# Performance work log

Hardware: AMD Instinct MI355X
Metric: run time of the kernel (lower is better)

## Reference

```python
import jax, jax.numpy as jnp
import numpy as np

N = 50000   # nodes
E = 800000  # edges (avg degree 16)
F_IN = 128
H = 128
L = 4
LN_EPS = 1e-5


def setup_inputs() -> dict:
    key = jax.random.key(0)
    ks = jax.random.split(key, 4)
    x = jax.random.normal(ks[0], (N, F_IN), dtype=jnp.float32)
    edge_index = jax.random.randint(ks[1], (2, E), 0, N)
    conv_w = jax.random.normal(ks[2], (L, F_IN, H), dtype=jnp.float32) * 0.05
    conv_b = jnp.zeros((L, H), dtype=jnp.float32)
    ln_g = jnp.ones((L, H), dtype=jnp.float32)
    ln_b = jnp.zeros((L, H), dtype=jnp.float32)
    head_w = jax.random.normal(ks[3], (H, 1), dtype=jnp.float32) * 0.05
    head_b = jnp.zeros((1,), dtype=jnp.float32)
    return {"x": x, "edge_index": edge_index, "conv_w": conv_w, "conv_b": conv_b,
            "ln_g": ln_g, "ln_b": ln_b, "head_w": head_w, "head_b": head_b}


def _layer_norm(h, g, b):
    mu = jnp.mean(h, axis=-1, keepdims=True)
    var = jnp.mean(jnp.square(h - mu), axis=-1, keepdims=True)
    return (h - mu) * jax.lax.rsqrt(var + LN_EPS) * g + b


def _gcn_conv(h, W, b, src, dst, inv_sqrt_deg, inv_deg):
    # PyG GCNConv: self-loops + symmetric normalization D^-1/2 (A+I) D^-1/2, then bias.
    hw = h @ W  # (N, H)
    norm = inv_sqrt_deg[src] * inv_sqrt_deg[dst]  # (E,)
    msg = hw[src] * norm[:, None]  # gather + edgewise scale
    agg = jax.ops.segment_sum(msg, dst, num_segments=N)  # scatter-add
    agg = agg + hw * inv_deg[:, None]  # self-loop term (norm = 1/deg)
    return agg + b


def reference(x, edge_index, conv_w, conv_b, ln_g, ln_b, head_w, head_b):
    src, dst = edge_index[0], edge_index[1]
    # degree on target nodes, including self-loop
    deg = jax.ops.segment_sum(jnp.ones((E,), x.dtype), dst, num_segments=N) + 1.0
    inv_sqrt_deg = jax.lax.rsqrt(deg)
    inv_deg = 1.0 / deg
    h = x
    for i in range(L):
        h = _gcn_conv(h, conv_w[i], conv_b[i], src, dst, inv_sqrt_deg, inv_deg)
        h = _layer_norm(h, ln_g[i], ln_b[i])
        if i != L - 1:
            h = jax.nn.gelu(h, approximate=False)
            # dropout is identity in eval mode
    scores = (h @ head_w + head_b).squeeze(-1)  # (N,)
    return scores, h
```

## Files before the change

kernel.cpp:

```cpp
#include <hip/hip_runtime.h>
#include <math.h>

#define N_NODES 50000
#define N_EDGES 800000
#define HDIM 128
#define NLAYERS 4
#define LN_EPS 1e-5f
#define EQUARTER (N_EDGES / 4)
#define SEG 64
#define FILLB ((EQUARTER + 255) / 256)
#define GEMMB ((N_NODES + 63) / 64)
#define LFB ((N_NODES + 31) / 32)

typedef __attribute__((ext_vector_type(8))) short short8;
typedef __attribute__((ext_vector_type(4))) float floatx4;

__device__ __forceinline__ ushort f2bf(float x) {
    unsigned b = __float_as_uint(x);
    unsigned r = b + 0x7fffu + ((b >> 16) & 1u);
    return (ushort)(r >> 16);
}
__device__ __forceinline__ float2 bf2f2(unsigned u) {
    return make_float2(__uint_as_float(u << 16), __uint_as_float(u & 0xffff0000u));
}


__device__ __forceinline__ void fill_body(int bid, int tid, const int* __restrict__ src,
                                          const int* __restrict__ dst, int* __restrict__ cnt,
                                          ushort* __restrict__ csr16) {
    int t = bid * 256 + tid;
    if (t >= EQUARTER) return;
    int s0 = src[t],                d0 = dst[t];
    int s1 = src[t + EQUARTER],     d1 = dst[t + EQUARTER];
    int s2 = src[t + 2 * EQUARTER], d2 = dst[t + 2 * EQUARTER];
    int s3 = src[t + 3 * EQUARTER], d3 = dst[t + 3 * EQUARTER];
    int p0 = atomicAdd(&cnt[d0], 1);
    int p1 = atomicAdd(&cnt[d1], 1);
    int p2 = atomicAdd(&cnt[d2], 1);
    int p3 = atomicAdd(&cnt[d3], 1);
    if (p0 < SEG) csr16[d0 * SEG + p0] = (ushort)s0;
    if (p1 < SEG) csr16[d1 * SEG + p1] = (ushort)s1;
    if (p2 < SEG) csr16[d2 * SEG + p2] = (ushort)s2;
    if (p3 < SEG) csr16[d3 * SEG + p3] = (ushort)s3;
}

__global__ __launch_bounds__(256) void isd_kernel(const int* __restrict__ cnt,
                                                  float* __restrict__ isd,
                                                  float* __restrict__ ind) {
    int i = blockIdx.x * 256 + threadIdx.x;
    if (i < N_NODES) {
        float d = (float)cnt[i] + 1.0f;
        isd[i] = rsqrtf(d);
        ind[i] = 1.0f / d;
    }
}

__global__ __launch_bounds__(256) void bprep_kernel(const float* __restrict__ W,
                                                    ushort* __restrict__ bfrag) {
    int idx = blockIdx.x * 256 + threadIdx.x;
    if (idx >= NLAYERS * 4 * 8 * 64) return;
    int lane = idx & 63;
    int t = (idx >> 6) & 7;
    int s = (idx >> 9) & 3;
    int l = idx >> 11;
    int n = t * 16 + (lane & 15);
    int kb = s * 32 + (lane >> 4) * 8;
    const float* Wl = W + (size_t)l * HDIM * HDIM;
    union { uint4 q; ushort u[8]; } o;
#pragma unroll
    for (int j = 0; j < 8; ++j) o.u[j] = f2bf(Wl[(size_t)(kb + j) * HDIM + n]);
    *(uint4*)&bfrag[(size_t)idx * 8] = o.q;
}

template <bool A_FP32>
__device__ __forceinline__ void gemm_body(int bid, int tid, const void* __restrict__ Av,
                                          const ushort* __restrict__ bfrag,
                                          ushort* __restrict__ out) {
    int wave = tid >> 6, lane = tid & 63;
    int quad = lane >> 4, mrow = lane & 15;
    int rowBase = bid * 64 + wave * 16;
    int arow = rowBase + mrow;
    bool aok = arow < N_NODES;

    floatx4 acc[8];
#pragma unroll
    for (int t = 0; t < 8; ++t) acc[t] = (floatx4)0.f;

#pragma unroll
    for (int s = 0; s < 4; ++s) {
        union { short8 v; ushort u[8]; } af;
        if (A_FP32) {
            const float* A = (const float*)Av;
            if (aok) {
                const float* p = &A[(size_t)arow * HDIM + s * 32 + quad * 8];
#pragma unroll
                for (int j = 0; j < 8; ++j) af.u[j] = f2bf(p[j]);
            } else {
#pragma unroll
                for (int j = 0; j < 8; ++j) af.u[j] = 0;
            }
        } else {
            const ushort* A = (const ushort*)Av;
            if (aok) {
                af.v = *(const short8*)&A[(size_t)arow * HDIM + s * 32 + quad * 8];
            } else {
#pragma unroll
                for (int j = 0; j < 8; ++j) af.u[j] = 0;
            }
        }
#pragma unroll
        for (int t = 0; t < 8; ++t) {
            short8 bf = *(const short8*)&bfrag[(size_t)(((s * 8 + t) * 64) + lane) * 8];
            acc[t] = __builtin_amdgcn_mfma_f32_16x16x32_bf16(af.v, bf, acc[t], 0, 0, 0);
        }
    }
#pragma unroll
    for (int t = 0; t < 8; ++t) {
#pragma unroll
        for (int r = 0; r < 4; ++r) {
            int row = rowBase + quad * 4 + r;
            if (row < N_NODES) out[(size_t)row * HDIM + t * 16 + mrow] = f2bf(acc[t][r]);
        }
    }
}

__global__ __launch_bounds__(256) void fused0_kernel(
    const int* __restrict__ src, const int* __restrict__ dst, int* __restrict__ cnt,
    ushort* __restrict__ csr16, const float* __restrict__ x,
    const ushort* __restrict__ bfrag0, ushort* __restrict__ hw) {
    if (blockIdx.x < FILLB)
        fill_body(blockIdx.x, threadIdx.x, src, dst, cnt, csr16);
    else
        gemm_body<true>(blockIdx.x - FILLB, threadIdx.x, x, bfrag0, hw);
}

__global__ __launch_bounds__(256) void agg_ln_kernel(
    const uint2* __restrict__ hw2, const int* __restrict__ degcnt,
    const ushort* __restrict__ csr16, const float* __restrict__ isd,
    const float* __restrict__ ind, const float* __restrict__ conv_b,
    const float* __restrict__ ln_g, const float* __restrict__ ln_b,
    uint2* __restrict__ hout_bf, float* __restrict__ hout_f32,
    const float* __restrict__ head_w, const float* __restrict__ head_b,
    float* __restrict__ scores, int final_layer) {
    int wave = threadIdx.x >> 6;
    int lane = threadIdx.x & 63;
    int g = lane >> 5;
    int li = lane & 31;
    int n = blockIdx.x * 4 + wave;
    if (n >= N_NODES) return;
    int c = li * 4;

    float isd_n = isd[n], ind_n = ind[n];
    int rs = n * SEG;
    int deg = min(degcnt[n], SEG);

    float e0 = 0.f, e1 = 0.f, e2 = 0.f, e3 = 0.f;
    int sj = 0;
    float wj = 0.f;
    if (lane < deg) {
        sj = (int)csr16[rs + lane];
        wj = isd[sj];
    }
    for (int j = 0; j < deg; j += 8) {
#pragma unroll
        for (int t = 0; t < 4; ++t) {
            int idx = j + 2 * t + g;
            int s = __shfl(sj, idx);
            float w = __shfl(wj, idx);
            uint2 u = hw2[(size_t)s * 32 + li];
            float2 q0 = bf2f2(u.x), q1 = bf2f2(u.y);
            e0 = fmaf(q0.x, w, e0); e1 = fmaf(q0.y, w, e1);
            e2 = fmaf(q1.x, w, e2); e3 = fmaf(q1.y, w, e3);
        }
    }
    e0 += __shfl_xor(e0, 32); e1 += __shfl_xor(e1, 32);
    e2 += __shfl_xor(e2, 32); e3 += __shfl_xor(e3, 32);

    uint2 hv = hw2[(size_t)n * 32 + li];
    float2 h0 = bf2f2(hv.x), h1 = bf2f2(hv.y);
    float4 cb = *(const float4*)&conv_b[c];
    float a0 = fmaf(e0, isd_n, fmaf(h0.x, ind_n, cb.x));
    float a1 = fmaf(e1, isd_n, fmaf(h0.y, ind_n, cb.y));
    float a2 = fmaf(e2, isd_n, fmaf(h1.x, ind_n, cb.z));
    float a3 = fmaf(e3, isd_n, fmaf(h1.y, ind_n, cb.w));

    float sum = a0 + a1 + a2 + a3;
#pragma unroll
    for (int o = 1; o < 32; o <<= 1) sum += __shfl_xor(sum, o);
    float mu = sum * (1.0f / HDIM);
    float d0 = a0 - mu, d1 = a1 - mu, d2 = a2 - mu, d3 = a3 - mu;
    float vs = d0 * d0 + d1 * d1 + d2 * d2 + d3 * d3;
#pragma unroll
    for (int o = 1; o < 32; o <<= 1) vs += __shfl_xor(vs, o);
    float rstd = rsqrtf(vs * (1.0f / HDIM) + LN_EPS);
    float4 gv = *(const float4*)&ln_g[c];
    float4 bv = *(const float4*)&ln_b[c];
    float y0 = fmaf(d0 * rstd, gv.x, bv.x);
    float y1 = fmaf(d1 * rstd, gv.y, bv.y);
    float y2 = fmaf(d2 * rstd, gv.z, bv.z);
    float y3 = fmaf(d3 * rstd, gv.w, bv.w);

    if (!final_layer) {
#define GELU(v) ((v) = 0.5f * (v) * (1.0f + erff((v) * 0.70710678118654752f)))
        GELU(y0); GELU(y1); GELU(y2); GELU(y3);
#undef GELU
        if (g == 0) {
            uint2 ov;
            ov.x = (unsigned)f2bf(y0) | ((unsigned)f2bf(y1) << 16);
            ov.y = (unsigned)f2bf(y2) | ((unsigned)f2bf(y3) << 16);
            hout_bf[(size_t)n * 32 + li] = ov;
        }
    } else {
        if (g == 0)
            *(float4*)&hout_f32[(size_t)n * HDIM + c] = make_float4(y0, y1, y2, y3);
        float4 hwv = *(const float4*)&head_w[c];
        float p = y0 * hwv.x + y1 * hwv.y + y2 * hwv.z + y3 * hwv.w;
#pragma unroll
        for (int o = 1; o < 32; o <<= 1) p += __shfl_xor(p, o);
        if (lane == 0) scores[n] = p + head_b[0];
    }
}

__global__ __launch_bounds__(512) void layer_fused_kernel(
    const uint2* __restrict__ h2, const int* __restrict__ degcnt,
    const ushort* __restrict__ csr16, const float* __restrict__ isd,
    const float* __restrict__ ind, const ushort* __restrict__ bfrag,
    const float* __restrict__ conv_b, const float* __restrict__ ln_g,
    const float* __restrict__ ln_b, uint2* __restrict__ hout_bf,
    float* __restrict__ hout_f32, const float* __restrict__ head_w,
    const float* __restrict__ head_b, float* __restrict__ scores,
    int final_layer) {
    __shared__ float aggsf[32][132];
    int wave = threadIdx.x >> 6, lane = threadIdx.x & 63;
    int g = lane >> 5, li = lane & 31;

    int nodeBase = blockIdx.x * 32 + wave * 4;
    int deg_c = 0, sj_c = 0;
    float wj_c = 0.f;
    if (nodeBase < N_NODES) {
        deg_c = min(degcnt[nodeBase], SEG);
        int sraw = (int)csr16[nodeBase * SEG + lane];
        sj_c = (lane < deg_c) ? sraw : 0;
        float w = isd[sj_c];
        wj_c = (lane < deg_c) ? w : 0.f;
    }
    for (int it = 0; it < 4; ++it) {
        int n = nodeBase + it;
        int deg = deg_c, sj = sj_c;
        float wj = wj_c;
        int deg_nx = 0, sraw_nx = 0;
        if (it < 3 && (n + 1) < N_NODES) {
            deg_nx = min(degcnt[n + 1], SEG);
            sraw_nx = (int)csr16[(n + 1) * SEG + lane];
        }
        float a0 = 0.f, a1 = 0.f, a2 = 0.f, a3 = 0.f;
        if (n < N_NODES) {
            float isd_n = isd[n], ind_n = ind[n];
            uint2 hv = h2[(size_t)n * 32 + li];
            float e0 = 0.f, e1 = 0.f, e2 = 0.f, e3 = 0.f;
            uint2 u[4];
#pragma unroll
            for (int t = 0; t < 4; ++t) {
                int s = __shfl(sj, 2 * t + g);
                u[t] = h2[(size_t)s * 32 + li];
            }
            for (int j = 0; j < deg; j += 8) {
                uint2 un[4];
                int jn = j + 8;
                bool more = jn < deg;
                if (more) {
#pragma unroll
                    for (int t = 0; t < 4; ++t) {
                        int s = __shfl(sj, jn + 2 * t + g);
                        un[t] = h2[(size_t)s * 32 + li];
                    }
                }
#pragma unroll
                for (int t = 0; t < 4; ++t) {
                    float w = __shfl(wj, j + 2 * t + g);
                    float2 q0 = bf2f2(u[t].x), q1 = bf2f2(u[t].y);
                    e0 = fmaf(q0.x, w, e0); e1 = fmaf(q0.y, w, e1);
                    e2 = fmaf(q1.x, w, e2); e3 = fmaf(q1.y, w, e3);
                }
                if (more) { u[0] = un[0]; u[1] = un[1]; u[2] = un[2]; u[3] = un[3]; }
            }
            e0 += __shfl_xor(e0, 32); e1 += __shfl_xor(e1, 32);
            e2 += __shfl_xor(e2, 32); e3 += __shfl_xor(e3, 32);
            float2 h0 = bf2f2(hv.x), h1v = bf2f2(hv.y);
            a0 = fmaf(e0, isd_n, h0.x * ind_n);
            a1 = fmaf(e1, isd_n, h0.y * ind_n);
            a2 = fmaf(e2, isd_n, h1v.x * ind_n);
            a3 = fmaf(e3, isd_n, h1v.y * ind_n);
        }
        if (g == 0)
            *(float4*)&aggsf[wave * 4 + it][li * 4] = make_float4(a0, a1, a2, a3);
        deg_c = deg_nx;
        sj_c = (lane < deg_nx) ? sraw_nx : 0;
        float w = isd[sj_c];
        wj_c = (lane < deg_nx) ? w : 0.f;
    }
    __syncthreads();

    int quad = lane >> 4, mrow = lane & 15;
    int rtile = (wave >> 2) * 16;
    int cq2 = (wave & 3) * 2;
    floatx4 acc[2];
    acc[0] = (floatx4)0.f;
    acc[1] = (floatx4)0.f;
#pragma unroll
    for (int s = 0; s < 4; ++s) {
        const float* rowp = &aggsf[rtile + mrow][s * 32 + quad * 8];
        float4 pa = *(const float4*)rowp;
        float4 pb = *(const float4*)(rowp + 4);
        float p[8] = {pa.x, pa.y, pa.z, pa.w, pb.x, pb.y, pb.z, pb.w};
        union { short8 v; ushort u[8]; } hi, lo;
#pragma unroll
        for (int j = 0; j < 8; ++j) {
            ushort h = f2bf(p[j]);
            hi.u[j] = h;
            float hf = __uint_as_float((unsigned)h << 16);
            lo.u[j] = f2bf(p[j] - hf);
        }
#pragma unroll
        for (int t4 = 0; t4 < 2; ++t4) {
            int t = cq2 + t4;
            short8 bf = *(const short8*)&bfrag[(size_t)(((s * 8 + t) * 64) + lane) * 8];
            acc[t4] = __builtin_amdgcn_mfma_f32_16x16x32_bf16(lo.v, bf, acc[t4], 0, 0, 0);
            acc[t4] = __builtin_amdgcn_mfma_f32_16x16x32_bf16(hi.v, bf, acc[t4], 0, 0, 0);
        }
    }
    __syncthreads();

    {
        float cb[2];
#pragma unroll
        for (int t4 = 0; t4 < 2; ++t4) cb[t4] = conv_b[(cq2 + t4) * 16 + mrow];
#pragma unroll
        for (int t4 = 0; t4 < 2; ++t4)
#pragma unroll
            for (int r = 0; r < 4; ++r)
                aggsf[rtile + quad * 4 + r][(cq2 + t4) * 16 + mrow] = acc[t4][r] + cb[t4];
    }
    __syncthreads();

    int c = li * 4;
    float4 gv = *(const float4*)&ln_g[c];
    float4 bv = *(const float4*)&ln_b[c];
    float4 hwv = *(const float4*)&head_w[c];
    for (int it = 0; it < 4; ++it) {
        int row = wave * 4 + it;
        int n = blockIdx.x * 32 + row;
        if (n >= N_NODES) continue;
        float4 v = *(const float4*)&aggsf[row][c];
        float a0 = v.x, a1 = v.y, a2 = v.z, a3 = v.w;

        float sum = a0 + a1 + a2 + a3;
#pragma unroll
        for (int o = 1; o < 32; o <<= 1) sum += __shfl_xor(sum, o);
        float mu = sum * (1.0f / HDIM);
        float d0 = a0 - mu, d1 = a1 - mu, d2 = a2 - mu, d3 = a3 - mu;
        float vs = d0 * d0 + d1 * d1 + d2 * d2 + d3 * d3;
#pragma unroll
        for (int o = 1; o < 32; o <<= 1) vs += __shfl_xor(vs, o);
        float rstd = rsqrtf(vs * (1.0f / HDIM) + LN_EPS);
        float y0 = fmaf(d0 * rstd, gv.x, bv.x);
        float y1 = fmaf(d1 * rstd, gv.y, bv.y);
        float y2 = fmaf(d2 * rstd, gv.z, bv.z);
        float y3 = fmaf(d3 * rstd, gv.w, bv.w);

        if (!final_layer) {
#define GELU(v) ((v) = 0.5f * (v) * (1.0f + erff((v) * 0.70710678118654752f)))
            GELU(y0); GELU(y1); GELU(y2); GELU(y3);
#undef GELU
            if (g == 0) {
                uint2 ov;
                ov.x = (unsigned)f2bf(y0) | ((unsigned)f2bf(y1) << 16);
                ov.y = (unsigned)f2bf(y2) | ((unsigned)f2bf(y3) << 16);
                hout_bf[(size_t)n * 32 + li] = ov;
            }
        } else {
            if (g == 0)
                *(float4*)&hout_f32[(size_t)n * HDIM + c] = make_float4(y0, y1, y2, y3);
            float p = y0 * hwv.x + y1 * hwv.y + y2 * hwv.z + y3 * hwv.w;
#pragma unroll
            for (int o = 1; o < 32; o <<= 1) p += __shfl_xor(p, o);
            if (lane == 0) scores[n] = p + head_b[0];
        }
    }
}


extern "C" void kernel_launch(void* const* d_in, const int* in_sizes, int n_in,
                              void* d_out, int out_size, void* d_ws, size_t ws_size,
                              hipStream_t stream) {
    const float* x      = (const float*)d_in[0];
    const int*   eidx   = (const int*)d_in[1];
    const float* conv_w = (const float*)d_in[2];
    const float* conv_b = (const float*)d_in[3];
    const float* ln_g   = (const float*)d_in[4];
    const float* ln_b   = (const float*)d_in[5];
    const float* head_w = (const float*)d_in[6];
    const float* head_b = (const float*)d_in[7];
    float* out = (float*)d_out;

    const int* src = eidx;
    const int* dst = eidx + N_EDGES;

    char* ws = (char*)d_ws;
    size_t o = 0;
    auto alloc = [&](size_t elems) {
        void* p = ws + o * 4;
        o += (elems + 15) & ~(size_t)15;
        return p;
    };
    int*      cnt      = (int*)alloc(N_NODES);
    float*    isd      = (float*)alloc(N_NODES);
    float*    ind      = (float*)alloc(N_NODES);
    ushort*   csr16    = (ushort*)alloc((size_t)N_NODES * SEG / 2);
    ushort*   bfrag    = (ushort*)alloc(NLAYERS * 4 * 8 * 64 * 8 / 2);
    unsigned* hw       = (unsigned*)alloc((size_t)N_NODES * 64);
    unsigned* hbuf     = (unsigned*)alloc((size_t)N_NODES * 64);

    hipMemsetAsync(cnt, 0, N_NODES * sizeof(int), stream);
    bprep_kernel<<<(NLAYERS * 4 * 8 * 64 + 255) / 256, 256, 0, stream>>>(conv_w, bfrag);
    fused0_kernel<<<FILLB + GEMMB, 256, 0, stream>>>(src, dst, cnt, csr16, x, bfrag,
                                                     (ushort*)hw);
    isd_kernel<<<(N_NODES + 255) / 256, 256, 0, stream>>>(cnt, isd, ind);

    agg_ln_kernel<<<(N_NODES + 3) / 4, 256, 0, stream>>>(
        (const uint2*)hw, cnt, csr16, isd, ind,
        conv_b, ln_g, ln_b,
        (uint2*)hbuf, out + N_NODES, head_w, head_b, out, 0);

    const unsigned* hin = hbuf;
    unsigned* hnext = hw;
    for (int l = 1; l < NLAYERS; ++l) {
        const ushort* bl = bfrag + (size_t)l * 4 * 8 * 64 * 8;
        int fin = (l == NLAYERS - 1) ? 1 : 0;
        layer_fused_kernel<<<LFB, 512, 0, stream>>>(
            (const uint2*)hin, cnt, csr16, isd, ind, bl,
            conv_b + (size_t)l * HDIM, ln_g + (size_t)l * HDIM, ln_b + (size_t)l * HDIM,
            (uint2*)hnext, out + N_NODES, head_w, head_b, out, fin);
        const unsigned* tmp = hin;
        hin = hnext;
        hnext = (unsigned*)tmp;
    }
}
```

Before: 361.9 us.

## Fold memset and degree-norm kernels into prep and consumers, recompute rsqrt inline

Merges the memset of the count array with the weight-fragment prep kernel and removes the separate isd/ind kernel. The aggregation kernels now compute the inverse square root of degree directly from the raw counts. The edge-fill loop is also changed from four edges per thread to two. This cuts two launches and the isd/ind arrays, at the cost of extra rsqrt work in each layer's aggregation.

```diff
diff --git a/kernel.cpp b/kernel.cpp
--- a/kernel.cpp
+++ b/kernel.cpp
@@ -6,9 +6,9 @@
 #define HDIM 128
 #define NLAYERS 4
 #define LN_EPS 1e-5f
-#define EQUARTER (N_EDGES / 4)
+#define EHALF (N_EDGES / 2)
 #define SEG 64
-#define FILLB ((EQUARTER + 255) / 256)
+#define FILLB ((EHALF + 255) / 256)
 #define GEMMB ((N_NODES + 63) / 64)
 #define LFB ((N_NODES + 31) / 32)
 
@@ -24,52 +24,37 @@
     return make_float2(__uint_as_float(u << 16), __uint_as_float(u & 0xffff0000u));
 }
 
+__global__ __launch_bounds__(256) void prep_kernel(const float* __restrict__ W,
+                                                   ushort* __restrict__ bfrag,
+                                                   int* __restrict__ cnt) {
+    int idx = blockIdx.x * 256 + threadIdx.x;
+    if (idx < N_NODES) cnt[idx] = 0;
+    if (idx < NLAYERS * 4 * 8 * 64) {
+        int lane = idx & 63;
+        int t = (idx >> 6) & 7;
+        int s = (idx >> 9) & 3;
+        int l = idx >> 11;
+        int n = t * 16 + (lane & 15);
+        int kb = s * 32 + (lane >> 4) * 8;
+        const float* Wl = W + (size_t)l * HDIM * HDIM;
+        union { uint4 q; ushort u[8]; } o;
+#pragma unroll
+        for (int j = 0; j < 8; ++j) o.u[j] = f2bf(Wl[(size_t)(kb + j) * HDIM + n]);
+        *(uint4*)&bfrag[(size_t)idx * 8] = o.q;
+    }
+}
 
 __device__ __forceinline__ void fill_body(int bid, int tid, const int* __restrict__ src,
                                           const int* __restrict__ dst, int* __restrict__ cnt,
                                           ushort* __restrict__ csr16) {
     int t = bid * 256 + tid;
-    if (t >= EQUARTER) return;
-    int s0 = src[t],                d0 = dst[t];
-    int s1 = src[t + EQUARTER],     d1 = dst[t + EQUARTER];
-    int s2 = src[t + 2 * EQUARTER], d2 = dst[t + 2 * EQUARTER];
-    int s3 = src[t + 3 * EQUARTER], d3 = dst[t + 3 * EQUARTER];
+    if (t >= EHALF) return;
+    int s0 = src[t],         d0 = dst[t];
+    int s1 = src[t + EHALF], d1 = dst[t + EHALF];
     int p0 = atomicAdd(&cnt[d0], 1);
     int p1 = atomicAdd(&cnt[d1], 1);
-    int p2 = atomicAdd(&cnt[d2], 1);
-    int p3 = atomicAdd(&cnt[d3], 1);
     if (p0 < SEG) csr16[d0 * SEG + p0] = (ushort)s0;
     if (p1 < SEG) csr16[d1 * SEG + p1] = (ushort)s1;
-    if (p2 < SEG) csr16[d2 * SEG + p2] = (ushort)s2;
-    if (p3 < SEG) csr16[d3 * SEG + p3] = (ushort)s3;
-}
-
-__global__ __launch_bounds__(256) void isd_kernel(const int* __restrict__ cnt,
-                                                  float* __restrict__ isd,
-                                                  float* __restrict__ ind) {
-    int i = blockIdx.x * 256 + threadIdx.x;
-    if (i < N_NODES) {
-        float d = (float)cnt[i] + 1.0f;
-        isd[i] = rsqrtf(d);
-        ind[i] = 1.0f / d;
-    }
-}
-
-__global__ __launch_bounds__(256) void bprep_kernel(const float* __restrict__ W,
-                                                    ushort* __restrict__ bfrag) {
-    int idx = blockIdx.x * 256 + threadIdx.x;
-    if (idx >= NLAYERS * 4 * 8 * 64) return;
-    int lane = idx & 63;
-    int t = (idx >> 6) & 7;
-    int s = (idx >> 9) & 3;
-    int l = idx >> 11;
-    int n = t * 16 + (lane & 15);
-    int kb = s * 32 + (lane >> 4) * 8;
-    const float* Wl = W + (size_t)l * HDIM * HDIM;
-    union { uint4 q; ushort u[8]; } o;
-#pragma unroll
-    for (int j = 0; j < 8; ++j) o.u[j] = f2bf(Wl[(size_t)(kb + j) * HDIM + n]);
-    *(uint4*)&bfrag[(size_t)idx * 8] = o.q;
 }
 
 template <bool A_FP32>
@@ -136,8 +121,7 @@
 
 __global__ __launch_bounds__(256) void agg_ln_kernel(
     const uint2* __restrict__ hw2, const int* __restrict__ degcnt,
-    const ushort* __restrict__ csr16, const float* __restrict__ isd,
-    const float* __restrict__ ind, const float* __restrict__ conv_b,
+    const ushort* __restrict__ csr16, const float* __restrict__ conv_b,
     const float* __restrict__ ln_g, const float* __restrict__ ln_b,
     uint2* __restrict__ hout_bf, float* __restrict__ hout_f32,
     const float* __restrict__ head_w, const float* __restrict__ head_b,
@@ -150,16 +134,20 @@
     if (n >= N_NODES) return;
     int c = li * 4;
 
-    float isd_n = isd[n], ind_n = ind[n];
+    int rawc = degcnt[n];
+    float dsum = (float)rawc + 1.0f;
+    float isd_n = rsqrtf(dsum);
+    float ind_n = isd_n * isd_n;
     int rs = n * SEG;
-    int deg = min(degcnt[n], SEG);
+    int deg = min(rawc, SEG);
 
     float e0 = 0.f, e1 = 0.f, e2 = 0.f, e3 = 0.f;
     int sj = 0;
     float wj = 0.f;
-    if (lane < deg) {
-        sj = (int)csr16[rs + lane];
-        wj = isd[sj];
+    if (lane < deg) sj = (int)csr16[rs + lane];
+    {
+        float w = rsqrtf((float)degcnt[sj] + 1.0f);
+        wj = (lane < deg) ? w : 0.f;
     }
     for (int j = 0; j < deg; j += 8) {
 #pragma unroll
@@ -223,8 +211,7 @@
 
 __global__ __launch_bounds__(512) void layer_fused_kernel(
     const uint2* __restrict__ h2, const int* __restrict__ degcnt,
-    const ushort* __restrict__ csr16, const float* __restrict__ isd,
-    const float* __restrict__ ind, const ushort* __restrict__ bfrag,
+    const ushort* __restrict__ csr16, const ushort* __restrict__ bfrag,
     const float* __restrict__ conv_b, const float* __restrict__ ln_g,
     const float* __restrict__ ln_b, uint2* __restrict__ hout_bf,
     float* __restrict__ hout_f32, const float* __restrict__ head_w,
@@ -235,27 +222,30 @@
     int g = lane >> 5, li = lane & 31;
 
     int nodeBase = blockIdx.x * 32 + wave * 4;
-    int deg_c = 0, sj_c = 0;
+    int cnt_c = 0, sj_c = 0;
     float wj_c = 0.f;
     if (nodeBase < N_NODES) {
-        deg_c = min(degcnt[nodeBase], SEG);
+        cnt_c = degcnt[nodeBase];
+        int degp = min(cnt_c, SEG);
         int sraw = (int)csr16[nodeBase * SEG + lane];
-        sj_c = (lane < deg_c) ? sraw : 0;
-        float w = isd[sj_c];
-        wj_c = (lane < deg_c) ? w : 0.f;
+        sj_c = (lane < degp) ? sraw : 0;
+        float w = rsqrtf((float)degcnt[sj_c] + 1.0f);
+        wj_c = (lane < degp) ? w : 0.f;
     }
     for (int it = 0; it < 4; ++it) {
         int n = nodeBase + it;
-        int deg = deg_c, sj = sj_c;
+        int deg = min(cnt_c, SEG), sj = sj_c;
+        float dsum = (float)cnt_c + 1.0f;
         float wj = wj_c;
-        int deg_nx = 0, sraw_nx = 0;
+        int cnt_nx = 0, sraw_nx = 0;
         if (it < 3 && (n + 1) < N_NODES) {
-            deg_nx = min(degcnt[n + 1], SEG);
+            cnt_nx = degcnt[n + 1];
             sraw_nx = (int)csr16[(n + 1) * SEG + lane];
         }
         float a0 = 0.f, a1 = 0.f, a2 = 0.f, a3 = 0.f;
         if (n < N_NODES) {
-            float isd_n = isd[n], ind_n = ind[n];
+            float isd_n = rsqrtf(dsum);
+            float ind_n = isd_n * isd_n;
             uint2 hv = h2[(size_t)n * 32 + li];
             float e0 = 0.f, e1 = 0.f, e2 = 0.f, e3 = 0.f;
             uint2 u[4];
@@ -294,10 +284,11 @@
         }
         if (g == 0)
             *(float4*)&aggsf[wave * 4 + it][li * 4] = make_float4(a0, a1, a2, a3);
-        deg_c = deg_nx;
-        sj_c = (lane < deg_nx) ? sraw_nx : 0;
-        float w = isd[sj_c];
-        wj_c = (lane < deg_nx) ? w : 0.f;
+        int degp = min(cnt_nx, SEG);
+        cnt_c = cnt_nx;
+        sj_c = (lane < degp) ? sraw_nx : 0;
+        float w = rsqrtf((float)degcnt[sj_c] + 1.0f);
+        wj_c = (lane < degp) ? w : 0.f;
     }
     __syncthreads();
 
@@ -414,21 +405,17 @@
         return p;
     };
     int*      cnt      = (int*)alloc(N_NODES);
-    float*    isd      = (float*)alloc(N_NODES);
-    float*    ind      = (float*)alloc(N_NODES);
     ushort*   csr16    = (ushort*)alloc((size_t)N_NODES * SEG / 2);
     ushort*   bfrag    = (ushort*)alloc(NLAYERS * 4 * 8 * 64 * 8 / 2);
     unsigned* hw       = (unsigned*)alloc((size_t)N_NODES * 64);
     unsigned* hbuf     = (unsigned*)alloc((size_t)N_NODES * 64);
 
-    hipMemsetAsync(cnt, 0, N_NODES * sizeof(int), stream);
-    bprep_kernel<<<(NLAYERS * 4 * 8 * 64 + 255) / 256, 256, 0, stream>>>(conv_w, bfrag);
+    prep_kernel<<<(N_NODES + 255) / 256, 256, 0, stream>>>(conv_w, bfrag, cnt);
     fused0_kernel<<<FILLB + GEMMB, 256, 0, stream>>>(src, dst, cnt, csr16, x, bfrag,
                                                      (ushort*)hw);
-    isd_kernel<<<(N_NODES + 255) / 256, 256, 0, stream>>>(cnt, isd, ind);
 
     agg_ln_kernel<<<(N_NODES + 3) / 4, 256, 0, stream>>>(
-        (const uint2*)hw, cnt, csr16, isd, ind,
+        (const uint2*)hw, cnt, csr16,
         conv_b, ln_g, ln_b,
         (uint2*)hbuf, out + N_NODES, head_w, head_b, out, 0);
 
@@ -438,7 +425,7 @@
         const ushort* bl = bfrag + (size_t)l * 4 * 8 * 64 * 8;
         int fin = (l == NLAYERS - 1) ? 1 : 0;
         layer_fused_kernel<<<LFB, 512, 0, stream>>>(
-            (const uint2*)hin, cnt, csr16, isd, ind, bl,
+            (const uint2*)hin, cnt, csr16, bl,
             conv_b + (size_t)l * HDIM, ln_g + (size_t)l * HDIM, ln_b + (size_t)l * HDIM,
             (uint2*)hnext, out + N_NODES, head_w, head_b, out, fin);
         const unsigned* tmp = hin;
```

New measurement: 340.2 us. 6.0% less time.
